# Kernel optimization log

Measured on AMD Instinct MI355X. Metric: run time of the kernel, lower is better.

Reference implementation:

```python
import jax, jax.numpy as jnp
import numpy as np

DEPTH = 128
NEG_MAX = -jnp.finfo(jnp.float32).max


def setup_inputs() -> dict:
    key = jax.random.key(0)
    ks = jax.random.split(key, 10)
    B, S, F, C = 16, 2048, 512, 1000
    x = jax.random.normal(ks[0], (B, S, F), dtype=jnp.float32)
    attention_mask = jax.random.randint(ks[1], (B, S, S), 0, 2) == 1
    s = 1.0 / np.sqrt(F)
    Wq = jax.random.uniform(ks[2], (F, DEPTH), jnp.float32, -s, s)
    bq = jax.random.uniform(ks[3], (DEPTH,), jnp.float32, -s, s)
    Wk = jax.random.uniform(ks[4], (F, DEPTH), jnp.float32, -s, s)
    bk = jax.random.uniform(ks[5], (DEPTH,), jnp.float32, -s, s)
    Wv = jax.random.uniform(ks[6], (F, DEPTH), jnp.float32, -s, s)
    bv = jax.random.uniform(ks[7], (DEPTH,), jnp.float32, -s, s)
    sl = 1.0 / np.sqrt(DEPTH)
    Wl = jax.random.uniform(ks[8], (DEPTH, C), jnp.float32, -sl, sl)
    bl = jax.random.uniform(ks[9], (C,), jnp.float32, -sl, sl)
    return {"x": x, "attention_mask": attention_mask,
            "Wq": Wq, "bq": bq, "Wk": Wk, "bk": bk,
            "Wv": Wv, "bv": bv, "Wl": Wl, "bl": bl}


def reference(x, attention_mask, Wq, bq, Wk, bk, Wv, bv, Wl, bl):
    # x: [B, S, F]; single-head attention with depth=128
    q = (x @ Wq + bq) * (DEPTH ** -0.5)          # [B, S, D] (is_scaled_dot_product)
    k = x @ Wk + bk                               # [B, S, D]
    v = x @ Wv + bv                               # [B, S, D]
    logit = jnp.einsum('bsd,btd->bst', q, k)      # [B, S, S]
    # masked_fill_(mask, -float_max) then added to logits
    logit = logit + jnp.where(attention_mask, NEG_MAX, 0.0)
    attn = jax.nn.softmax(logit, axis=2)
    out = jnp.einsum('bst,btd->bsd', attn, v)     # [B, S, D]
    out = out @ Wl + bl                           # [B, S, C]
    return out.mean(axis=1)                       # [B, C]
```

## Files before the change

kernel.cpp:

```cpp
#include <hip/hip_runtime.h>
#include <stdint.h>

#define BB 16
#define SS 2048
#define FF 512
#define DD 128
#define CC 1000

typedef __attribute__((ext_vector_type(8))) short bf16x8;
typedef __attribute__((ext_vector_type(4))) float f32x4;

__device__ __forceinline__ unsigned short f2bf(float f) {
  unsigned x;
  __builtin_memcpy(&x, &f, 4);
  x = x + 0x7FFFu + ((x >> 16) & 1u);
  return (unsigned short)(x >> 16);
}
__device__ __forceinline__ float bf2f(unsigned short u) {
  unsigned x = ((unsigned)u) << 16;
  float f;
  __builtin_memcpy(&f, &x, 4);
  return f;
}
__device__ __forceinline__ unsigned pk2(float a, float b) {
  return (unsigned)f2bf(a) | ((unsigned)f2bf(b) << 16);
}

#define WS_WG   256
#define WS_ZG   131328
#define WS_YG   262400
#define WS_PK   270592
#define WS_Q    8659200
#define WS_K    17047808
#define WS_V    25436416
#define WS_WT   33825024
#define WS_END  34218240
#define WS_P    34218240
#define WS_END2 168435968

__global__ __launch_bounds__(256) void k_detect(const unsigned* __restrict__ mask,
                                                int* __restrict__ flags,
                                                float* __restrict__ wgl,
                                                float* __restrict__ zgl,
                                                float* __restrict__ ygl) {
  __shared__ unsigned red;
  const int tid = threadIdx.x;
  if (tid == 0) red = 0;
  __syncthreads();
  unsigned a = 0;
#pragma unroll
  for (int j = 0; j < 4; ++j) a |= mask[tid * 4 + j] & 0xFFFFFF00u;
  if (a) atomicOr(&red, 1u);
  __syncthreads();
  if (tid == 0) flags[0] = (red == 0) ? 1 : 0;
  for (int i = tid; i < BB * SS; i += 256) { wgl[i] = 0.f; zgl[i] = 0.f; }
  for (int i = tid; i < BB * DD; i += 256) ygl[i] = 0.f;
}

__global__ __launch_bounds__(256) void k_pack(const void* __restrict__ mask,
                                              const int* __restrict__ flags,
                                              unsigned* __restrict__ pk) {
  const int tid = threadIdx.x;
  const long long base = (long long)blockIdx.x * 2048;
  const bool isInt = flags[0] != 0;
#pragma unroll
  for (int it = 0; it < 8; ++it) {
    long long e = base + it * 256 + tid;
    int val;
    if (isInt) val = ((const int*)mask)[e];
    else       val = ((const unsigned char*)mask)[e];
    unsigned long long bal = __ballot(val != 0);
    if ((tid & 31) == 0)
      pk[e >> 5] = (unsigned)((tid & 63) ? (bal >> 32) : bal);
  }
}

__global__ __launch_bounds__(256) void k_wt(const float* __restrict__ Wq,
                                            const float* __restrict__ Wk,
                                            const float* __restrict__ Wv,
                                            unsigned short* __restrict__ wt) {
  int idx = blockIdx.x * 256 + threadIdx.x;
  int ty = idx >> 16;
  int o = idx & 65535;
  int d = o >> 9, f = o & 511;
  const float* W = ty == 0 ? Wq : (ty == 1 ? Wk : Wv);
  wt[idx] = f2bf(W[f * DD + d]);
}

__global__ __launch_bounds__(256) void k_proj(const float* __restrict__ xg,
                                              const unsigned short* __restrict__ wtg,
                                              const float* __restrict__ bq,
                                              const float* __restrict__ bk,
                                              const float* __restrict__ bv,
                                              unsigned short* __restrict__ qo,
                                              unsigned short* __restrict__ ko,
                                              unsigned short* __restrict__ vo) {
  __shared__ __align__(16) char lA[8192];
  __shared__ __align__(16) char lB[8192];
  const int tid = threadIdx.x;
  const int lane = tid & 63;
  const int wv = tid >> 6;
  const int colL = lane & 15, quad = lane >> 4;
  const int blk = blockIdx.x, ty = blockIdx.y;
  const float* bias = ty == 0 ? bq : (ty == 1 ? bk : bv);
  unsigned short* outp = ty == 0 ? qo : (ty == 1 ? ko : vo);
  const float scale = ty == 0 ? 0.08838834764831845f : 1.0f;
  const unsigned short* wbase = wtg + (size_t)ty * 65536;
  const int m0 = (wv & 1) * 64, n0 = (wv >> 1) * 64;

  f32x4 acc[4][4];
  const f32x4 z4 = {0.f, 0.f, 0.f, 0.f};
#pragma unroll
  for (int mi = 0; mi < 4; ++mi)
#pragma unroll
    for (int ni = 0; ni < 4; ++ni) acc[mi][ni] = z4;

  for (int ic = 0; ic < 16; ++ic) {
    const int k0 = ic * 32;
    uint4 va[2], vb[2];
#pragma unroll
    for (int rr = 0; rr < 2; ++rr) {
      int p = rr * 256 + tid;
      int row = p >> 2, c = p & 3;
      const float* xp = xg + (size_t)(blk * 128 + row) * FF + k0 + c * 8;
      float4 x0 = *(const float4*)xp;
      float4 x1 = *(const float4*)(xp + 4);
      va[rr].x = pk2(x0.x, x0.y); va[rr].y = pk2(x0.z, x0.w);
      va[rr].z = pk2(x1.x, x1.y); va[rr].w = pk2(x1.z, x1.w);
      vb[rr] = *(const uint4*)(wbase + (size_t)row * FF + k0 + c * 8);
    }
    __syncthreads();
#pragma unroll
    for (int rr = 0; rr < 2; ++rr) {
      int p = rr * 256 + tid;
      int row = p >> 2, c = p & 3;
      int phys = c ^ ((row >> 1) & 3);
      *(uint4*)(lA + row * 64 + phys * 16) = va[rr];
      *(uint4*)(lB + row * 64 + phys * 16) = vb[rr];
    }
    __syncthreads();
    bf16x8 af[4], bfr[4];
#pragma unroll
    for (int mi = 0; mi < 4; ++mi) {
      int ar = m0 + mi * 16 + colL;
      int phys = quad ^ ((ar >> 1) & 3);
      af[mi] = *(const bf16x8*)(lA + ar * 64 + phys * 16);
    }
#pragma unroll
    for (int ni = 0; ni < 4; ++ni) {
      int br = n0 + ni * 16 + colL;
      int phys = quad ^ ((br >> 1) & 3);
      bfr[ni] = *(const bf16x8*)(lB + br * 64 + phys * 16);
    }
#pragma unroll
    for (int mi = 0; mi < 4; ++mi)
#pragma unroll
      for (int ni = 0; ni < 4; ++ni)
        acc[mi][ni] = __builtin_amdgcn_mfma_f32_16x16x32_bf16(af[mi], bfr[ni], acc[mi][ni], 0, 0, 0);
  }
#pragma unroll
  for (int ni = 0; ni < 4; ++ni) {
    int col = n0 + ni * 16 + colL;
    float bval = bias[col];
#pragma unroll
    for (int mi = 0; mi < 4; ++mi) {
#pragma unroll
      for (int r = 0; r < 4; ++r) {
        int row = blk * 128 + m0 + mi * 16 + quad * 4 + r;
        float val = (acc[mi][ni][r] + bval) * scale;
        outp[(size_t)row * DD + col] = f2bf(val);
      }
    }
  }
}

template <int MODE>
__global__ __launch_bounds__(256) void k_attn2(const unsigned short* __restrict__ qg,
                                               const unsigned short* __restrict__ kg,
                                               const unsigned* __restrict__ pk,
                                               float* __restrict__ zg,
                                               float* __restrict__ wg,
                                               unsigned short* __restrict__ pg) {
  __shared__ __align__(16) char kt[16384];
  __shared__ unsigned maskt[128 * 9];
  __shared__ float wacc[256];
  const int tid = threadIdx.x;
  const int lane = tid & 63, wv = tid >> 6;
  const int colL = lane & 15, quad = lane >> 4;
  const int row0 = blockIdx.x * 128;
  const int tc = blockIdx.y;
  const int b = blockIdx.z;
  const int tbase = tc * 256;

  for (int i = tid; i < 1024; i += 256) {
    int row = i >> 3, w = i & 7;
    maskt[row * 9 + w] = pk[((size_t)b * SS + row0 + row) * 64 + tc * 8 + w];
  }
  if (MODE == 2) wacc[tid] = 0.f;

  bf16x8 qf[2][4];
#pragma unroll
  for (int mi = 0; mi < 2; ++mi) {
    int qrow = row0 + wv * 32 + mi * 16 + colL;
    const unsigned short* qp = qg + ((size_t)b * SS + qrow) * DD + quad * 8;
#pragma unroll
    for (int kk = 0; kk < 4; ++kk) qf[mi][kk] = *(const bf16x8*)(qp + kk * 32);
  }
  float z[2][4] = {{0.f, 0.f, 0.f, 0.f}, {0.f, 0.f, 0.f, 0.f}};
  float zinv[2][4];
  if (MODE == 2) {
#pragma unroll
    for (int mi = 0; mi < 2; ++mi)
#pragma unroll
      for (int r = 0; r < 4; ++r) {
        int row = row0 + wv * 32 + mi * 16 + quad * 4 + r;
        zinv[mi][r] = 1.0f / fmaxf(zg[(size_t)b * SS + row], 1e-30f);
      }
  }

  for (int kt0 = 0; kt0 < 4; ++kt0) {
    const int t0 = tbase + kt0 * 64;
    uint4 kreg[4];
#pragma unroll
    for (int rr = 0; rr < 4; ++rr) {
      int p = rr * 256 + tid;
      int row = p >> 4, c = p & 15;
      kreg[rr] = *(const uint4*)(kg + ((size_t)b * SS + t0 + row) * DD + c * 8);
    }
    __syncthreads();
#pragma unroll
    for (int rr = 0; rr < 4; ++rr) {
      int p = rr * 256 + tid;
      int row = p >> 4, c = p & 15;
      int phys = c ^ (row & 7);
      *(uint4*)(kt + row * 256 + phys * 16) = kreg[rr];
    }
    __syncthreads();
#pragma unroll
    for (int nt = 0; nt < 4; ++nt) {
      int rb = nt * 16 + colL;
      bf16x8 bb[4];
#pragma unroll
      for (int kk = 0; kk < 4; ++kk) {
        int phys = (kk * 4 + quad) ^ (rb & 7);
        bb[kk] = *(const bf16x8*)(kt + rb * 256 + phys * 16);
      }
      int tl = kt0 * 64 + nt * 16 + colL;
      int wl = tl >> 5, wb = tl & 31;
      float cs = 0.f;
#pragma unroll
      for (int mi = 0; mi < 2; ++mi) {
        f32x4 acc = {0.f, 0.f, 0.f, 0.f};
        acc = __builtin_amdgcn_mfma_f32_16x16x32_bf16(qf[mi][0], bb[0], acc, 0, 0, 0);
        acc = __builtin_amdgcn_mfma_f32_16x16x32_bf16(qf[mi][1], bb[1], acc, 0, 0, 0);
        acc = __builtin_amdgcn_mfma_f32_16x16x32_bf16(qf[mi][2], bb[2], acc, 0, 0, 0);
        acc = __builtin_amdgcn_mfma_f32_16x16x32_bf16(qf[mi][3], bb[3], acc, 0, 0, 0);
        int rbase = wv * 32 + mi * 16 + quad * 4;
        unsigned short* pp;
        if (MODE == 1)
          pp = pg + ((size_t)b * SS + row0 + rbase) * SS + tbase + tl;
#pragma unroll
        for (int r = 0; r < 4; ++r) {
          unsigned mw = maskt[(rbase + r) * 9 + wl];
          float e = ((mw >> wb) & 1u) ? 0.f : __expf(fminf(acc[r], 80.f));
          if (MODE != 2) z[mi][r] += e;
          else cs += e * zinv[mi][r];
          if (MODE == 1) pp[(size_t)r * SS] = f2bf(e);
        }
      }
      if (MODE == 2) {
        cs += __shfl_xor(cs, 16, 64);
        cs += __shfl_xor(cs, 32, 64);
        if (quad == 0) atomicAdd(&wacc[tl], cs);
      }
    }
  }
  if (MODE != 2) {
#pragma unroll
    for (int mi = 0; mi < 2; ++mi)
#pragma unroll
      for (int r = 0; r < 4; ++r) {
        float s = z[mi][r];
        s += __shfl_xor(s, 1, 64);
        s += __shfl_xor(s, 2, 64);
        s += __shfl_xor(s, 4, 64);
        s += __shfl_xor(s, 8, 64);
        if (colL == 0) {
          int row = row0 + wv * 32 + mi * 16 + quad * 4 + r;
          atomicAdd(&zg[(size_t)b * SS + row], s);
        }
      }
  } else {
    __syncthreads();
    atomicAdd(&wg[(size_t)b * SS + tbase + tid], wacc[tid]);
  }
}

__global__ __launch_bounds__(256) void k_csum(const unsigned short* __restrict__ pg,
                                              const float* __restrict__ zg,
                                              float* __restrict__ wg) {
  __shared__ float zl[64];
  const int tid = threadIdx.x;
  const int s0 = blockIdx.x * 64;
  const int b = blockIdx.y;
  if (tid < 64) zl[tid] = 1.0f / fmaxf(zg[(size_t)b * SS + s0 + tid], 1e-30f);
  __syncthreads();
  float acc[8] = {0.f, 0.f, 0.f, 0.f, 0.f, 0.f, 0.f, 0.f};
  const unsigned short* base = pg + ((size_t)b * SS + s0) * SS + tid * 8;
#pragma unroll 4
  for (int s = 0; s < 64; ++s) {
    bf16x8 pv = *(const bf16x8*)(base + (size_t)s * SS);
    float zi = zl[s];
#pragma unroll
    for (int j = 0; j < 8; ++j) acc[j] += bf2f((unsigned short)pv[j]) * zi;
  }
  float* wrow = wg + (size_t)b * SS + tid * 8;
#pragma unroll
  for (int j = 0; j < 8; ++j) atomicAdd(&wrow[j], acc[j]);
}

__global__ __launch_bounds__(256) void k_yv(const float* __restrict__ wgl,
                                            const unsigned short* __restrict__ vg,
                                            float* __restrict__ ygl) {
  const int tid = threadIdx.x;
  const int tc = blockIdx.x, b = blockIdx.y;
  const int d = tid & 127, half = tid >> 7;
  const int t0 = tc * 128 + half * 64;
  float p = 0.f;
  const float* wrow = wgl + (size_t)b * SS + t0;
  const unsigned short* vrow = vg + ((size_t)b * SS + t0) * DD + d;
#pragma unroll 8
  for (int t = 0; t < 64; ++t) p += wrow[t] * bf2f(vrow[(size_t)t * DD]);
  atomicAdd(&ygl[b * DD + d], p);
}

__global__ __launch_bounds__(256) void k_out(const float* __restrict__ ygl,
                                             const float* __restrict__ Wl,
                                             const float* __restrict__ bl,
                                             float* __restrict__ outp) {
  __shared__ float ys[DD];
  const int tid = threadIdx.x;
  const int b = blockIdx.x;
  if (tid < DD) ys[tid] = ygl[b * DD + tid] * (1.0f / 2048.0f);
  __syncthreads();
  for (int c = tid; c < CC; c += 256) {
    float a = bl[c];
#pragma unroll 16
    for (int dd = 0; dd < DD; ++dd) a += ys[dd] * Wl[dd * CC + c];
    outp[b * CC + c] = a;
  }
}

extern "C" void kernel_launch(void* const* d_in, const int* in_sizes, int n_in,
                              void* d_out, int out_size, void* d_ws, size_t ws_size,
                              hipStream_t stream) {
  const void* ptr[10];
  for (int i = 0; i < 10; ++i) ptr[i] = (i < n_in) ? d_in[i] : nullptr;
  if (n_in == 10) {
    const void *px = 0, *pm = 0, *pWl = 0, *pbl = 0;
    const void* pW[3] = {0, 0, 0};
    const void* pb[3] = {0, 0, 0};
    int nW = 0, nb = 0;
    for (int i = 0; i < 10; ++i) {
      int s = in_sizes[i];
      if (s == 16777216) px = d_in[i];
      else if (s == 67108864) pm = d_in[i];
      else if (s == 128000) pWl = d_in[i];
      else if (s == 1000) pbl = d_in[i];
      else if (s == 65536 && nW < 3) pW[nW++] = d_in[i];
      else if (s == 128 && nb < 3) pb[nb++] = d_in[i];
    }
    if (px && pm && pWl && pbl && nW == 3 && nb == 3) {
      ptr[0] = px; ptr[1] = pm;
      ptr[2] = pW[0]; ptr[3] = pb[0];
      ptr[4] = pW[1]; ptr[5] = pb[1];
      ptr[6] = pW[2]; ptr[7] = pb[2];
      ptr[8] = pWl; ptr[9] = pbl;
    }
  }
  char* ws = (char*)d_ws;
  if (ws_size < (size_t)WS_END) return;
  int* flags = (int*)ws;
  float* wg = (float*)(ws + WS_WG);
  float* zg = (float*)(ws + WS_ZG);
  float* yg = (float*)(ws + WS_YG);
  unsigned* pk = (unsigned*)(ws + WS_PK);
  unsigned short* q  = (unsigned short*)(ws + WS_Q);
  unsigned short* k  = (unsigned short*)(ws + WS_K);
  unsigned short* v  = (unsigned short*)(ws + WS_V);
  unsigned short* wt = (unsigned short*)(ws + WS_WT);
  unsigned short* pbuf = (unsigned short*)(ws + WS_P);
  const bool bigws = ws_size >= (size_t)WS_END2;

  k_detect<<<1, 256, 0, stream>>>((const unsigned*)ptr[1], flags, wg, zg, yg);
  k_pack<<<32768, 256, 0, stream>>>(ptr[1], flags, pk);
  k_wt<<<768, 256, 0, stream>>>((const float*)ptr[2], (const float*)ptr[4],
                                (const float*)ptr[6], wt);
  k_proj<<<dim3(256, 3), 256, 0, stream>>>((const float*)ptr[0], wt,
                                           (const float*)ptr[3], (const float*)ptr[5],
                                           (const float*)ptr[7], q, k, v);
  if (bigws) {
    k_attn2<1><<<dim3(16, 8, 16), 256, 0, stream>>>(q, k, pk, zg, wg, pbuf);
    k_csum<<<dim3(32, 16), 256, 0, stream>>>(pbuf, zg, wg);
  } else {
    k_attn2<0><<<dim3(16, 8, 16), 256, 0, stream>>>(q, k, pk, zg, wg, nullptr);
    k_attn2<2><<<dim3(16, 8, 16), 256, 0, stream>>>(q, k, pk, zg, wg, nullptr);
  }
  k_yv<<<dim3(16, 16), 256, 0, stream>>>(wg, v, yg);
  k_out<<<16, 256, 0, stream>>>(yg, (const float*)ptr[8], (const float*)ptr[9],
                                (float*)d_out);
}
```

Before: 635.3 us.

## Merge detect into weight transpose, coarsen pack/csum, stage P tile through LDS

Folds the mask-type detection and accumulator zeroing into the weight-transpose kernel as an extra block, removing one launch. The mask-pack kernel processes sixteen times more elements per block with fewer blocks, and the column-sum kernel handles 256 rows per block, cutting global atomics. The attention kernel now buffers exponentiated probabilities in a swizzled LDS tile and writes them out as coalesced 16-byte rows instead of scattered 2-byte stores. The exchange is extra LDS use and a barrier per key tile, plus less parallelism in the pack and csum grids.

```diff
diff --git a/kernel.cpp b/kernel.cpp
--- a/kernel.cpp
+++ b/kernel.cpp
@@ -38,33 +38,45 @@
 #define WS_P    34218240
 #define WS_END2 168435968
 
-__global__ __launch_bounds__(256) void k_detect(const unsigned* __restrict__ mask,
-                                                int* __restrict__ flags,
-                                                float* __restrict__ wgl,
-                                                float* __restrict__ zgl,
-                                                float* __restrict__ ygl) {
-  __shared__ unsigned red;
-  const int tid = threadIdx.x;
-  if (tid == 0) red = 0;
-  __syncthreads();
-  unsigned a = 0;
-#pragma unroll
-  for (int j = 0; j < 4; ++j) a |= mask[tid * 4 + j] & 0xFFFFFF00u;
-  if (a) atomicOr(&red, 1u);
-  __syncthreads();
-  if (tid == 0) flags[0] = (red == 0) ? 1 : 0;
-  for (int i = tid; i < BB * SS; i += 256) { wgl[i] = 0.f; zgl[i] = 0.f; }
-  for (int i = tid; i < BB * DD; i += 256) ygl[i] = 0.f;
+__global__ __launch_bounds__(256) void k_wt(const float* __restrict__ Wq,
+                                            const float* __restrict__ Wk,
+                                            const float* __restrict__ Wv,
+                                            unsigned short* __restrict__ wt,
+                                            const unsigned* __restrict__ mask,
+                                            int* __restrict__ flags,
+                                            float* __restrict__ wgl,
+                                            float* __restrict__ zgl,
+                                            float* __restrict__ ygl) {
+  const int tid = threadIdx.x;
+  if (blockIdx.x == 768) {
+    __shared__ unsigned red;
+    if (tid == 0) red = 0;
+    __syncthreads();
+    unsigned a = 0;
+#pragma unroll
+    for (int j = 0; j < 4; ++j) a |= mask[tid * 4 + j] & 0xFFFFFF00u;
+    if (a) atomicOr(&red, 1u);
+    __syncthreads();
+    if (tid == 0) flags[0] = (red == 0) ? 1 : 0;
+    for (int i = tid; i < BB * SS; i += 256) { wgl[i] = 0.f; zgl[i] = 0.f; }
+    for (int i = tid; i < BB * DD; i += 256) ygl[i] = 0.f;
+    return;
+  }
+  int idx = blockIdx.x * 256 + tid;
+  int ty = idx >> 16;
+  int o = idx & 65535;
+  int d = o >> 9, f = o & 511;
+  const float* W = ty == 0 ? Wq : (ty == 1 ? Wk : Wv);
+  wt[idx] = f2bf(W[f * DD + d]);
 }
 
 __global__ __launch_bounds__(256) void k_pack(const void* __restrict__ mask,
                                               const int* __restrict__ flags,
                                               unsigned* __restrict__ pk) {
   const int tid = threadIdx.x;
-  const long long base = (long long)blockIdx.x * 2048;
+  const long long base = (long long)blockIdx.x * 32768;
   const bool isInt = flags[0] != 0;
-#pragma unroll
-  for (int it = 0; it < 8; ++it) {
+  for (int it = 0; it < 128; ++it) {
     long long e = base + it * 256 + tid;
     int val;
     if (isInt) val = ((const int*)mask)[e];
@@ -73,18 +85,6 @@
     if ((tid & 31) == 0)
       pk[e >> 5] = (unsigned)((tid & 63) ? (bal >> 32) : bal);
   }
-}
-
-__global__ __launch_bounds__(256) void k_wt(const float* __restrict__ Wq,
-                                            const float* __restrict__ Wk,
-                                            const float* __restrict__ Wv,
-                                            unsigned short* __restrict__ wt) {
-  int idx = blockIdx.x * 256 + threadIdx.x;
-  int ty = idx >> 16;
-  int o = idx & 65535;
-  int d = o >> 9, f = o & 511;
-  const float* W = ty == 0 ? Wq : (ty == 1 ? Wk : Wv);
-  wt[idx] = f2bf(W[f * DD + d]);
 }
 
 __global__ __launch_bounds__(256) void k_proj(const float* __restrict__ xg,
@@ -184,6 +184,7 @@
   __shared__ __align__(16) char kt[16384];
   __shared__ unsigned maskt[128 * 9];
   __shared__ float wacc[256];
+  __shared__ __align__(16) unsigned short pt[128 * 64];
   const int tid = threadIdx.x;
   const int lane = tid & 63, wv = tid >> 6;
   const int colL = lane & 15, quad = lane >> 4;
@@ -196,7 +197,7 @@
     int row = i >> 3, w = i & 7;
     maskt[row * 9 + w] = pk[((size_t)b * SS + row0 + row) * 64 + tc * 8 + w];
   }
-  if (MODE == 2) wacc[tid] = 0.f;
+  if constexpr (MODE == 2) wacc[tid] = 0.f;
 
   bf16x8 qf[2][4];
 #pragma unroll
@@ -208,7 +209,7 @@
   }
   float z[2][4] = {{0.f, 0.f, 0.f, 0.f}, {0.f, 0.f, 0.f, 0.f}};
   float zinv[2][4];
-  if (MODE == 2) {
+  if constexpr (MODE == 2) {
 #pragma unroll
     for (int mi = 0; mi < 2; ++mi)
 #pragma unroll
@@ -246,6 +247,7 @@
         bb[kk] = *(const bf16x8*)(kt + rb * 256 + phys * 16);
       }
       int tl = kt0 * 64 + nt * 16 + colL;
+      int ct = nt * 16 + colL;
       int wl = tl >> 5, wb = tl & 31;
       float cs = 0.f;
 #pragma unroll
@@ -256,26 +258,37 @@
         acc = __builtin_amdgcn_mfma_f32_16x16x32_bf16(qf[mi][2], bb[2], acc, 0, 0, 0);
         acc = __builtin_amdgcn_mfma_f32_16x16x32_bf16(qf[mi][3], bb[3], acc, 0, 0, 0);
         int rbase = wv * 32 + mi * 16 + quad * 4;
-        unsigned short* pp;
-        if (MODE == 1)
-          pp = pg + ((size_t)b * SS + row0 + rbase) * SS + tbase + tl;
 #pragma unroll
         for (int r = 0; r < 4; ++r) {
           unsigned mw = maskt[(rbase + r) * 9 + wl];
           float e = ((mw >> wb) & 1u) ? 0.f : __expf(fminf(acc[r], 80.f));
-          if (MODE != 2) z[mi][r] += e;
+          if constexpr (MODE != 2) z[mi][r] += e;
           else cs += e * zinv[mi][r];
-          if (MODE == 1) pp[(size_t)r * SS] = f2bf(e);
+          if constexpr (MODE == 1) {
+            int rw = rbase + r;
+            pt[rw * 64 + (ct ^ ((rw & 7) << 3))] = f2bf(e);
+          }
         }
       }
-      if (MODE == 2) {
+      if constexpr (MODE == 2) {
         cs += __shfl_xor(cs, 16, 64);
         cs += __shfl_xor(cs, 32, 64);
         if (quad == 0) atomicAdd(&wacc[tl], cs);
       }
     }
-  }
-  if (MODE != 2) {
+    if constexpr (MODE == 1) {
+      __syncthreads();
+      unsigned short* prow = pg + ((size_t)b * SS + row0) * SS + t0;
+#pragma unroll
+      for (int i2 = 0; i2 < 4; ++i2) {
+        int ii = i2 * 256 + tid;
+        int rw = ii >> 3, c8 = ii & 7;
+        uint4 vv = *(const uint4*)(pt + rw * 64 + ((c8 ^ (rw & 7)) * 8));
+        *(uint4*)(prow + (size_t)rw * SS + c8 * 8) = vv;
+      }
+    }
+  }
+  if constexpr (MODE != 2) {
 #pragma unroll
     for (int mi = 0; mi < 2; ++mi)
 #pragma unroll
@@ -299,16 +312,16 @@
 __global__ __launch_bounds__(256) void k_csum(const unsigned short* __restrict__ pg,
                                               const float* __restrict__ zg,
                                               float* __restrict__ wg) {
-  __shared__ float zl[64];
-  const int tid = threadIdx.x;
-  const int s0 = blockIdx.x * 64;
+  __shared__ float zl[256];
+  const int tid = threadIdx.x;
+  const int s0 = blockIdx.x * 256;
   const int b = blockIdx.y;
-  if (tid < 64) zl[tid] = 1.0f / fmaxf(zg[(size_t)b * SS + s0 + tid], 1e-30f);
+  zl[tid] = 1.0f / fmaxf(zg[(size_t)b * SS + s0 + tid], 1e-30f);
   __syncthreads();
   float acc[8] = {0.f, 0.f, 0.f, 0.f, 0.f, 0.f, 0.f, 0.f};
   const unsigned short* base = pg + ((size_t)b * SS + s0) * SS + tid * 8;
 #pragma unroll 4
-  for (int s = 0; s < 64; ++s) {
+  for (int s = 0; s < 256; ++s) {
     bf16x8 pv = *(const bf16x8*)(base + (size_t)s * SS);
     float zi = zl[s];
 #pragma unroll
@@ -392,16 +405,16 @@
   unsigned short* pbuf = (unsigned short*)(ws + WS_P);
   const bool bigws = ws_size >= (size_t)WS_END2;
 
-  k_detect<<<1, 256, 0, stream>>>((const unsigned*)ptr[1], flags, wg, zg, yg);
-  k_pack<<<32768, 256, 0, stream>>>(ptr[1], flags, pk);
-  k_wt<<<768, 256, 0, stream>>>((const float*)ptr[2], (const float*)ptr[4],
-                                (const float*)ptr[6], wt);
+  k_wt<<<769, 256, 0, stream>>>((const float*)ptr[2], (const float*)ptr[4],
+                                (const float*)ptr[6], wt,
+                                (const unsigned*)ptr[1], flags, wg, zg, yg);
+  k_pack<<<2048, 256, 0, stream>>>(ptr[1], flags, pk);
   k_proj<<<dim3(256, 3), 256, 0, stream>>>((const float*)ptr[0], wt,
                                            (const float*)ptr[3], (const float*)ptr[5],
                                            (const float*)ptr[7], q, k, v);
   if (bigws) {
     k_attn2<1><<<dim3(16, 8, 16), 256, 0, stream>>>(q, k, pk, zg, wg, pbuf);
-    k_csum<<<dim3(32, 16), 256, 0, stream>>>(pbuf, zg, wg);
+    k_csum<<<dim3(8, 16), 256, 0, stream>>>(pbuf, zg, wg);
   } else {
     k_attn2<0><<<dim3(16, 8, 16), 256, 0, stream>>>(q, k, pk, zg, wg, nullptr);
     k_attn2<2><<<dim3(16, 8, 16), 256, 0, stream>>>(q, k, pk, zg, wg, nullptr);
```

Result: faster. 621.3 us (-2.2%).
